# Performance work log

Measured on AMD Instinct MI355X. Metric: run time of the kernel, lower is better.

## Reference

```python
import jax, jax.numpy as jnp
import numpy as np

B = 4; E_PER = 100_000; E = B * E_PER
N_NODES = 50_000; N_REL = 500; D = 64; D_LG = 256
K_PER_VI = 20; S_VI = E // K_PER_VI          # 20000 sorted vi segments
S_VJ_PER = 5_000; S_VJ = B * S_VJ_PER        # 20000 unsorted vj segments
N_MEM = 131_072
INTERACT = ((0, 3), (0, 2, 3), (0, 4), (0, 2, 4), (1, 3), (1, 2, 3), (1, 4), (1, 2, 4))


def _build_edges():
    rng = np.random.default_rng(0)
    idx_vi = np.repeat(np.arange(S_VI), K_PER_VI)          # sorted segment ids
    gpb = S_VI // B
    eg = idx_vi // gpb                                     # sorted by eg_idx too
    vi = rng.integers(0, N_NODES, S_VI)[idx_vi]
    idx_vj = np.empty(E, dtype=np.int64)
    for b in range(B):
        loc = np.concatenate([np.arange(S_VJ_PER), rng.integers(0, S_VJ_PER, E_PER - S_VJ_PER)])
        rng.shuffle(loc)
        idx_vj[b * E_PER:(b + 1) * E_PER] = b * S_VJ_PER + loc  # every group non-empty
    vj = rng.integers(0, N_NODES, S_VJ)[idx_vj]            # consistent (eg, vj) per group
    rel = rng.integers(0, N_REL, E)
    e2vi = rng.integers(0, N_MEM, E)
    e2vj = rng.integers(0, N_MEM, E)
    return np.stack([eg, vi, vj, rel, idx_vi, idx_vj, e2vi, e2vj], axis=1).astype(np.int32)


def setup_inputs() -> dict:
    key = jax.random.key(0)
    ks = jax.random.split(key, 10)
    return {
        "node_attention": jax.random.uniform(ks[0], (B, N_NODES), jnp.float32),
        "scanned_edges": jnp.asarray(_build_edges()),
        "edges_y": jax.random.uniform(ks[1], (E,), jnp.float32),
        "hidden_uncon": jax.random.normal(ks[2], (1, N_NODES, D_LG), jnp.float32),
        "hidden_con": jax.random.normal(ks[3], (N_MEM, D), jnp.float32),
        "Wc": jax.random.normal(ks[4], (D, D), jnp.float32) / np.sqrt(D).astype(np.float32),
        "bc": jnp.zeros((D,), jnp.float32),
        "Wu": jax.random.normal(ks[5], (D_LG, D), jnp.float32) / np.sqrt(D_LG).astype(np.float32),
        "bu": jnp.zeros((D,), jnp.float32),
        "rel_table": jax.random.normal(ks[6], (N_REL, D), jnp.float32) * 0.05,
        "ws": jax.random.normal(ks[7], (len(INTERACT), D), jnp.float32) / np.sqrt(float(len(INTERACT))).astype(np.float32) if False else jax.random.normal(ks[7], (len(INTERACT), D), jnp.float32) * (1.0 / np.sqrt(len(INTERACT)).astype(np.float32)),
        "fb": jnp.zeros((D,), jnp.float32),
        "out_w": jax.random.normal(ks[8], (D,), jnp.float32),
        "out_b": jnp.zeros((D,), jnp.float32),
        "n_vi_segments": S_VI,
        "n_vj_segments": S_VJ,
    }


def reference(node_attention, scanned_edges, edges_y, hidden_uncon, hidden_con,
              Wc, bc, Wu, bu, rel_table, ws, fb, out_w, out_b,
              n_vi_segments, n_vj_segments):
    eg, vi, vj, rel = (scanned_edges[:, i] for i in range(4))
    idx_vi, idx_vj, e2vi, e2vj = (scanned_edges[:, i] for i in range(4, 8))
    # projections (proj_con / proj_uncon, tanh Dense)
    hc = jnp.tanh(hidden_con @ Wc + bc)          # [N_MEM, D]
    hu = jnp.tanh(hidden_uncon @ Wu + bu)[0]     # [n_nodes, D]; batch_size==1 path of Node2Edge
    # Node2Edge gathers
    feats = (hc[e2vi], hu[vi], rel_table[rel], hc[e2vj], hu[vj])  # each [E, D]
    # F layer: weighted sum of elementwise interaction products
    out = fb
    for k, idxs in enumerate(INTERACT):
        x = feats[idxs[0]]
        for i in idxs[1:]:
            x = x * feats[i]
        out = out + x * ws[k]
    out = jax.nn.relu(out) * out_w + out_b
    logits = jnp.sum(out, axis=1)                # [E]
    # NeighborSoftmax at 'vi' (sorted segment softmax)
    m = jax.ops.segment_max(logits, idx_vi, num_segments=n_vi_segments)
    ex = jnp.exp(logits - m[idx_vi])
    den = jax.ops.segment_sum(ex, idx_vi, num_segments=n_vi_segments)
    transition = ex / den[idx_vi]
    # attention flow: gather source attention, weight, aggregate at vj
    trans_att = transition * node_attention[eg, vi] * edges_y
    aggr = jax.ops.segment_sum(trans_att, idx_vj, num_segments=n_vj_segments)
    b_g = jax.ops.segment_max(eg, idx_vj, num_segments=n_vj_segments)
    vj_g = jax.ops.segment_max(vj, idx_vj, num_segments=n_vj_segments)
    new_node_attention = jnp.zeros_like(node_attention).at[b_g, vj_g].add(aggr)
    return new_node_attention
```

## Files before the change

kernel.cpp:

```cpp
#include <hip/hip_runtime.h>
#include <hip/hip_bf16.h>
#include <type_traits>

#define D 64
#define KPER 20

typedef __attribute__((ext_vector_type(8))) short short8;
typedef __attribute__((ext_vector_type(4))) float floatx4;

__device__ __forceinline__ unsigned short f2bfu(float x) {
    __hip_bfloat16 h = __float2bfloat16(x);
    return *reinterpret_cast<unsigned short*>(&h);
}
__device__ __forceinline__ float bfu2f(unsigned short u) {
    return __uint_as_float(((unsigned)u) << 16);
}

__device__ __forceinline__ float fast_tanh(float x) {
    float xc = fminf(fmaxf(x, -15.f), 15.f);
    float e = __expf(2.f * xc);
    return 1.f - 2.f * __builtin_amdgcn_rcpf(1.f + e);
}

template<int CTRL>
__device__ __forceinline__ float dpp_add(float x) {
    int t = __builtin_amdgcn_update_dpp(0, __float_as_int(x), CTRL, 0xf, 0xf, true);
    return x + __int_as_float(t);
}
template<int CTRL>
__device__ __forceinline__ float dpp_max(float x) {
    int xi = __float_as_int(x);
    int t = __builtin_amdgcn_update_dpp(xi, xi, CTRL, 0xf, 0xf, false);
    return fmaxf(x, __int_as_float(t));
}
__device__ __forceinline__ float wave_sum_b(float x) {
    x = dpp_add<0x111>(x); x = dpp_add<0x112>(x);
    x = dpp_add<0x114>(x); x = dpp_add<0x118>(x);
    x = dpp_add<0x142>(x); x = dpp_add<0x143>(x);
    return __int_as_float(__builtin_amdgcn_readlane(__float_as_int(x), 63));
}
__device__ __forceinline__ float wave_max_b(float x) {
    x = dpp_max<0x111>(x); x = dpp_max<0x112>(x);
    x = dpp_max<0x114>(x); x = dpp_max<0x118>(x);
    x = dpp_max<0x142>(x); x = dpp_max<0x143>(x);
    return __int_as_float(__builtin_amdgcn_readlane(__float_as_int(x), 63));
}

template<int I, int N, typename F>
__device__ __forceinline__ void static_for(F&& f) {
    if constexpr (I < N) {
        f(std::integral_constant<int, I>{});
        static_for<I + 1, N>(f);
    }
}

template<int SLOT>
__device__ __forceinline__ int get_slot(int m0, int m1, int m2) {
    if constexpr (SLOT < 64)       return __builtin_amdgcn_readlane(m0, SLOT);
    else if constexpr (SLOT < 128) return __builtin_amdgcn_readlane(m1, SLOT - 64);
    else                           return __builtin_amdgcn_readlane(m2, SLOT - 128);
}

template<int K, int CTN>
__device__ __forceinline__ void proj_body(const float* __restrict__ h,
        const float* __restrict__ W, const float* __restrict__ b,
        unsigned short* __restrict__ out, int ct0, int rt0, int rtstride, int ntiles) {
    constexpr int KT = K / 32;
    int lane = threadIdx.x & 63;
    int m = lane & 15, quad = lane >> 4;
    short8 bfr[CTN][KT];
    #pragma unroll
    for (int ct = 0; ct < CTN; ++ct)
        #pragma unroll
        for (int kt = 0; kt < KT; ++kt)
            #pragma unroll
            for (int j = 0; j < 8; ++j)
                bfr[ct][kt][j] = (short)f2bfu(W[(size_t)(kt * 32 + quad * 8 + j) * 64 + (ct0 + ct) * 16 + m]);
    float bv[CTN];
    #pragma unroll
    for (int ct = 0; ct < CTN; ++ct) bv[ct] = b[(ct0 + ct) * 16 + m];
    for (int rt = rt0; rt < ntiles; rt += rtstride) {
        floatx4 acc[CTN];
        #pragma unroll
        for (int ct = 0; ct < CTN; ++ct) acc[ct] = floatx4{0.f, 0.f, 0.f, 0.f};
        const float* hrow = h + (size_t)(rt * 16 + m) * K + quad * 8;
        #pragma unroll
        for (int kt = 0; kt < KT; ++kt) {
            floatx4 a0 = *(const floatx4*)(hrow + kt * 32);
            floatx4 a1 = *(const floatx4*)(hrow + kt * 32 + 4);
            short8 af;
            af[0] = (short)f2bfu(a0[0]); af[1] = (short)f2bfu(a0[1]);
            af[2] = (short)f2bfu(a0[2]); af[3] = (short)f2bfu(a0[3]);
            af[4] = (short)f2bfu(a1[0]); af[5] = (short)f2bfu(a1[1]);
            af[6] = (short)f2bfu(a1[2]); af[7] = (short)f2bfu(a1[3]);
            #pragma unroll
            for (int ct = 0; ct < CTN; ++ct)
                acc[ct] = __builtin_amdgcn_mfma_f32_16x16x32_bf16(af, bfr[ct][kt], acc[ct], 0, 0, 0);
        }
        #pragma unroll
        for (int ct = 0; ct < CTN; ++ct) {
            int col = (ct0 + ct) * 16 + m;
            #pragma unroll
            for (int reg = 0; reg < 4; ++reg) {
                int row = rt * 16 + quad * 4 + reg;
                out[(size_t)row * 64 + col] = f2bfu(fast_tanh(acc[ct][reg] + bv[ct]));
            }
        }
    }
}

#define RELB 16
__global__ __launch_bounds__(256) void proj_fused(
        const float* __restrict__ hcon, const float* __restrict__ Wc, const float* __restrict__ bc,
        const float* __restrict__ hun, const float* __restrict__ Wu, const float* __restrict__ bu,
        const float* __restrict__ relf, unsigned short* __restrict__ hc,
        unsigned short* __restrict__ hu, unsigned short* __restrict__ relb,
        int t64, int t256, int g64, int g256, int nrel) {
    int bid = blockIdx.x;
    int w = threadIdx.x >> 6;
    if (bid < g64) {
        int wid = bid * 4 + w;
        proj_body<64, 4>(hcon, Wc, bc, hc, 0, wid, g64 * 4, t64);
    } else if (bid < g64 + g256) {
        int wid = (bid - g64) * 4 + w;
        int half = wid & 1;
        proj_body<256, 2>(hun, Wu, bu, hu, half * 2, wid >> 1, (g256 * 4) >> 1, t256);
    } else {
        int tid = (bid - g64 - g256) * 256 + threadIdx.x;
        for (int i = tid; i < nrel; i += RELB * 256) relb[i] = f2bfu(relf[i]);
    }
}

__global__ __launch_bounds__(256) void edge_kernel(
        const float* __restrict__ natt, const int* __restrict__ edges,
        const float* __restrict__ ey, const unsigned short* __restrict__ hc,
        const unsigned short* __restrict__ hu, const unsigned short* __restrict__ relt,
        const float* __restrict__ wsm, const float* __restrict__ fb,
        const float* __restrict__ outw, float* __restrict__ out, int N) {
    int lane = threadIdx.x & 63;
    int s = blockIdx.x * 4 + (threadIdx.x >> 6);
    long base = (long)s * KPER;
    const int* eb = edges + base * 8;
    int m0 = eb[lane];
    int m1 = eb[64 + lane];
    int m2 = (lane < 32) ? eb[128 + lane] : 0;
    int eg = get_slot<0>(m0, m1, m2);
    int vi = get_slot<1>(m0, m1, m2);
    float f1 = bfu2f(hu[(size_t)vi * D + lane]);
    float na = natt[(size_t)eg * N + vi];
    float w0 = wsm[0 * D + lane], w1 = wsm[1 * D + lane];
    float w2 = wsm[2 * D + lane], w3 = wsm[3 * D + lane];
    float w4 = wsm[4 * D + lane], w5 = wsm[5 * D + lane];
    float w6 = wsm[6 * D + lane], w7 = wsm[7 * D + lane];
    float fbv = fb[lane], owv = outw[lane];
    float myl = -INFINITY;
    int myvj = 0;
    static_for<0, KPER>([&](auto ec) {
        constexpr int e = decltype(ec)::value;
        int vj  = get_slot<e * 8 + 2>(m0, m1, m2);
        int rel = get_slot<e * 8 + 3>(m0, m1, m2);
        int evi = get_slot<e * 8 + 6>(m0, m1, m2);
        int evj = get_slot<e * 8 + 7>(m0, m1, m2);
        float F0 = bfu2f(hc[(size_t)evi * D + lane]);
        float F2 = bfu2f(relt[(size_t)rel * D + lane]);
        float F3 = bfu2f(hc[(size_t)evj * D + lane]);
        float F4 = bfu2f(hu[(size_t)vj * D + lane]);
        float t1 = fmaf(F2, w1, w0);
        float t2 = fmaf(F2, w5, w4);
        float t3 = fmaf(F2, w3, w2);
        float t4 = fmaf(F2, w7, w6);
        float u = fmaf(F0, t1, f1 * t2);
        float v = fmaf(F0, t3, f1 * t4);
        float o = fmaf(F3, u, fmaf(F4, v, fbv));
        o = fmaxf(o, 0.0f) * owv;
        float tot = wave_sum_b(o);
        bool mine = (lane == e);
        myl = mine ? tot : myl;
        myvj = mine ? vj : myvj;
    });
    float mx = wave_max_b(myl);
    float ex = __expf(myl - mx);
    float den = wave_sum_b(ex);
    if (lane < KPER) {
        float t = (ex / den) * na * ey[base + lane];
        atomicAdd(out + (size_t)eg * N + myvj, t);
    }
}

extern "C" void kernel_launch(void* const* d_in, const int* in_sizes, int n_in,
                              void* d_out, int out_size, void* d_ws, size_t ws_size,
                              hipStream_t stream) {
    const float* natt = (const float*)d_in[0];
    const int*   edges = (const int*)d_in[1];
    const float* ey   = (const float*)d_in[2];
    const float* hun  = (const float*)d_in[3];
    const float* hcon = (const float*)d_in[4];
    const float* Wc   = (const float*)d_in[5];
    const float* bc   = (const float*)d_in[6];
    const float* Wu   = (const float*)d_in[7];
    const float* bu   = (const float*)d_in[8];
    const float* relt = (const float*)d_in[9];
    const float* wsm  = (const float*)d_in[10];
    const float* fb   = (const float*)d_in[11];
    const float* outw = (const float*)d_in[12];
    float* out = (float*)d_out;

    int E    = in_sizes[2];
    int S    = E / KPER;
    int nmem = in_sizes[4] / D;
    int N    = in_sizes[3] / 256;
    int nrel = in_sizes[9];

    hipMemsetAsync(d_out, 0, (size_t)out_size * sizeof(float), stream);

    int t64  = nmem / 16;
    int t256 = N / 16;
    int g64  = 512, g256 = 512;

    unsigned short* hc = (unsigned short*)d_ws;
    unsigned short* hu = hc + (size_t)nmem * D;
    unsigned short* rb = hu + (size_t)N * D;

    proj_fused<<<g64 + g256 + RELB, 256, 0, stream>>>(hcon, Wc, bc, hun, Wu, bu,
                                                      relt, hc, hu, rb,
                                                      t64, t256, g64, g256, nrel);
    edge_kernel<<<S / 4, 256, 0, stream>>>(natt, edges, ey, hc, hu, rb,
                                           wsm, fb, outw, out, N);
}
```

Baseline: 207.2 us.

## Fold output zeroing into projection kernel and load edge indices via scalar loads

Removes the separate hipMemsetAsync and zeroes the output with extra blocks inside the projection kernel, which saves one launch. The edge kernel now makes the segment index wave-uniform with readfirstlane, so edge fields are read through scalar loads instead of vector loads followed by readlane. Edge kernel blocks grow from 4 to 8 waves. Scalar loads of 160 ints per wave could add latency before the gathers, since the earlier vector loads fetched all fields at once.

```diff
diff --git a/kernel.cpp b/kernel.cpp
--- a/kernel.cpp
+++ b/kernel.cpp
@@ -52,13 +52,6 @@
         f(std::integral_constant<int, I>{});
         static_for<I + 1, N>(f);
     }
-}
-
-template<int SLOT>
-__device__ __forceinline__ int get_slot(int m0, int m1, int m2) {
-    if constexpr (SLOT < 64)       return __builtin_amdgcn_readlane(m0, SLOT);
-    else if constexpr (SLOT < 128) return __builtin_amdgcn_readlane(m1, SLOT - 64);
-    else                           return __builtin_amdgcn_readlane(m2, SLOT - 128);
 }
 
 template<int K, int CTN>
@@ -110,11 +103,13 @@
 }
 
 #define RELB 16
+#define ZB 8
 __global__ __launch_bounds__(256) void proj_fused(
         const float* __restrict__ hcon, const float* __restrict__ Wc, const float* __restrict__ bc,
         const float* __restrict__ hun, const float* __restrict__ Wu, const float* __restrict__ bu,
         const float* __restrict__ relf, unsigned short* __restrict__ hc,
         unsigned short* __restrict__ hu, unsigned short* __restrict__ relb,
+        float* __restrict__ outz, int nout,
         int t64, int t256, int g64, int g256, int nrel) {
     int bid = blockIdx.x;
     int w = threadIdx.x >> 6;
@@ -125,27 +120,27 @@
         int wid = (bid - g64) * 4 + w;
         int half = wid & 1;
         proj_body<256, 2>(hun, Wu, bu, hu, half * 2, wid >> 1, (g256 * 4) >> 1, t256);
-    } else {
+    } else if (bid < g64 + g256 + RELB) {
         int tid = (bid - g64 - g256) * 256 + threadIdx.x;
         for (int i = tid; i < nrel; i += RELB * 256) relb[i] = f2bfu(relf[i]);
-    }
-}
-
-__global__ __launch_bounds__(256) void edge_kernel(
+    } else {
+        int tid = (bid - g64 - g256 - RELB) * 256 + threadIdx.x;
+        for (int i = tid; i < nout; i += ZB * 256) outz[i] = 0.0f;
+    }
+}
+
+__global__ __launch_bounds__(512) void edge_kernel(
         const float* __restrict__ natt, const int* __restrict__ edges,
         const float* __restrict__ ey, const unsigned short* __restrict__ hc,
         const unsigned short* __restrict__ hu, const unsigned short* __restrict__ relt,
         const float* __restrict__ wsm, const float* __restrict__ fb,
         const float* __restrict__ outw, float* __restrict__ out, int N) {
     int lane = threadIdx.x & 63;
-    int s = blockIdx.x * 4 + (threadIdx.x >> 6);
-    long base = (long)s * KPER;
+    int s = blockIdx.x * 8 + (threadIdx.x >> 6);
+    int su = __builtin_amdgcn_readfirstlane(s);
+    long base = (long)su * KPER;
     const int* eb = edges + base * 8;
-    int m0 = eb[lane];
-    int m1 = eb[64 + lane];
-    int m2 = (lane < 32) ? eb[128 + lane] : 0;
-    int eg = get_slot<0>(m0, m1, m2);
-    int vi = get_slot<1>(m0, m1, m2);
+    int eg = eb[0], vi = eb[1];
     float f1 = bfu2f(hu[(size_t)vi * D + lane]);
     float na = natt[(size_t)eg * N + vi];
     float w0 = wsm[0 * D + lane], w1 = wsm[1 * D + lane];
@@ -157,10 +152,10 @@
     int myvj = 0;
     static_for<0, KPER>([&](auto ec) {
         constexpr int e = decltype(ec)::value;
-        int vj  = get_slot<e * 8 + 2>(m0, m1, m2);
-        int rel = get_slot<e * 8 + 3>(m0, m1, m2);
-        int evi = get_slot<e * 8 + 6>(m0, m1, m2);
-        int evj = get_slot<e * 8 + 7>(m0, m1, m2);
+        int vj  = eb[e * 8 + 2];
+        int rel = eb[e * 8 + 3];
+        int evi = eb[e * 8 + 6];
+        int evj = eb[e * 8 + 7];
         float F0 = bfu2f(hc[(size_t)evi * D + lane]);
         float F2 = bfu2f(relt[(size_t)rel * D + lane]);
         float F3 = bfu2f(hc[(size_t)evj * D + lane]);
@@ -211,8 +206,6 @@
     int N    = in_sizes[3] / 256;
     int nrel = in_sizes[9];
 
-    hipMemsetAsync(d_out, 0, (size_t)out_size * sizeof(float), stream);
-
     int t64  = nmem / 16;
     int t256 = N / 16;
     int g64  = 512, g256 = 512;
@@ -221,9 +214,10 @@
     unsigned short* hu = hc + (size_t)nmem * D;
     unsigned short* rb = hu + (size_t)N * D;
 
-    proj_fused<<<g64 + g256 + RELB, 256, 0, stream>>>(hcon, Wc, bc, hun, Wu, bu,
-                                                      relt, hc, hu, rb,
-                                                      t64, t256, g64, g256, nrel);
-    edge_kernel<<<S / 4, 256, 0, stream>>>(natt, edges, ey, hc, hu, rb,
+    proj_fused<<<g64 + g256 + RELB + ZB, 256, 0, stream>>>(hcon, Wc, bc, hun, Wu, bu,
+                                                           relt, hc, hu, rb,
+                                                           out, out_size,
+                                                           t64, t256, g64, g256, nrel);
+    edge_kernel<<<S / 8, 512, 0, stream>>>(natt, edges, ey, hc, hu, rb,
                                            wsm, fb, outw, out, N);
 }
```

Measured after the change: 218.6 us. +5.5%, slower.
